# Kernel tuning notes

Measured on AMD Instinct MI355X. Metric: run time of the kernel, lower is better.

Reference implementation:

```python
import jax, jax.numpy as jnp
import numpy as np

B, Q, K, H = 8, 2048, 2048, 512


def setup_inputs() -> dict:
    key = jax.random.key(0)
    ks = jax.random.split(key, 12)
    s = 1.0 / np.sqrt(H)
    return {
        "query": jax.random.normal(ks[0], (B, Q, H), jnp.float32),
        "key_": jax.random.normal(ks[1], (B, K, H), jnp.float32),
        "value": jax.random.normal(ks[2], (B, K, H), jnp.float32),
        "mask": jax.random.randint(ks[3], (B, K), 0, 2).astype(bool),
        "Wq": jax.random.normal(ks[4], (H, H), jnp.float32) * s,
        "bq": jnp.zeros((H,), jnp.float32),
        "Wk": jax.random.normal(ks[5], (H, H), jnp.float32) * s,
        "bk": jnp.zeros((H,), jnp.float32),
        "Wv": jax.random.normal(ks[6], (H, H), jnp.float32) * s,
        "bv": jnp.zeros((H,), jnp.float32),
        "Wo": jax.random.normal(ks[7], (H, H), jnp.float32) * s,
        "bo": jnp.zeros((H,), jnp.float32),
    }


def reference(query, key_, value, mask, Wq, bq, Wk, bk, Wv, bv, Wo, bo):
    scale = jnp.sqrt(jnp.float32(H))
    Qp = query @ Wq + bq          # (B,Q,H)
    Kp = key_ @ Wk + bk           # (B,K,H)
    Vp = value @ Wv + bv          # (B,K,H)
    energy = jnp.einsum("bqh,bkh->bqk", Qp, Kp) / scale
    # mask is (B, key_len); torch code broadcasts it over all query rows
    energy = jnp.where(mask[:, None, :], -jnp.inf, energy)
    idx = jnp.argmax(energy, axis=-1)                 # (B,Q)
    score = jax.nn.one_hot(idx, K, dtype=energy.dtype)  # hardmax one-hot (B,Q,K)
    # score @ V is exactly a per-row gather of the argmax-selected V row
    res = jnp.take_along_axis(Vp, idx[:, :, None], axis=1)  # (B,Q,H)
    res = res @ Wo + bo
    return (res, score)
```

## Files before the change

kernel.cpp:

```cpp
#include <hip/hip_runtime.h>

typedef _Float16 f16;
typedef f16 f16x8 __attribute__((ext_vector_type(8)));
typedef f16 f16x4 __attribute__((ext_vector_type(4)));
typedef short s16x8 __attribute__((ext_vector_type(8)));
typedef short s16x4 __attribute__((ext_vector_type(4)));
typedef float f32x4 __attribute__((ext_vector_type(4)));

#define MFMA16(a,b,c)  __builtin_amdgcn_mfma_f32_16x16x32_f16(a,b,c,0,0,0)
#define MFMAB16(a,b,c) __builtin_amdgcn_mfma_f32_16x16x32_bf16(a,b,c,0,0,0)

static constexpr int Bn = 8, Qn = 2048, Kn = 2048, Hn = 512;
static constexpr int Mn = Bn * Qn;

typedef __attribute__((address_space(1))) const unsigned int as1_uint;
typedef __attribute__((address_space(3))) unsigned int as3_uint;

__device__ __forceinline__ void gl_lds16(const void* g, void* l) {
    __builtin_amdgcn_global_load_lds((as1_uint*)g, (as3_uint*)l, 16, 0, 0);
}

__device__ __forceinline__ short bf16r(float x) {
    unsigned u = __builtin_bit_cast(unsigned, x);
    u += 0x7fffu + ((u >> 16) & 1u);
    return (short)(u >> 16);
}

__device__ __forceinline__ int swz(int row) { return (row >> 1) & 3; }

__global__ __launch_bounds__(256) void compact_mask(
    const int* __restrict__ mask, int* __restrict__ cidx, int* __restrict__ cnt)
{
    __shared__ int sums[256];
    int b = blockIdx.x, t = threadIdx.x;
    int base = b * Kn + t * 8;
    int mv[8]; int s = 0;
    #pragma unroll
    for (int i = 0; i < 8; ++i) { mv[i] = (mask[base + i] == 0); s += mv[i]; }
    sums[t] = s;
    __syncthreads();
    for (int off = 1; off < 256; off <<= 1) {
        int v = (t >= off) ? sums[t - off] : 0;
        __syncthreads();
        sums[t] += v;
        __syncthreads();
    }
    int pos = (t > 0 ? sums[t - 1] : 0);
    #pragma unroll
    for (int i = 0; i < 8; ++i)
        if (mv[i]) cidx[b * Kn + pos++] = t * 8 + i;
    if (t == 255) {
        int total = sums[255];
        if (total == 0) { cidx[b * Kn] = 0; total = 1; }
        cnt[b] = total;
    }
}

__global__ __launch_bounds__(256) void prep_split(
    const float* __restrict__ Wk, const float* __restrict__ Wo,
    f16* __restrict__ Wk_h, f16* __restrict__ Wk_l, short* __restrict__ Wot)
{
    int e = blockIdx.x * 256 + threadIdx.x;
    float v = Wk[e] * 512.0f;
    f16 h = (f16)v;
    Wk_h[e] = h; Wk_l[e] = (f16)((v - (float)h) * 2048.0f);
    int r = e >> 9, c = e & 511;
    Wot[c * 512 + r] = bf16r(Wo[e]);
}

__global__ __launch_bounds__(512) void prep_vec(
    const float* __restrict__ Wk, const float* __restrict__ Wo,
    const float* __restrict__ bq, const float* __restrict__ bv,
    const float* __restrict__ bo,
    float* __restrict__ wvec, float* __restrict__ cvec)
{
    int t = threadIdx.x;
    float s = 0.f;
    for (int n = 0; n < 512; n += 4) {
        f32x4 a = *(const f32x4*)(Wk + (size_t)t * 512 + n);
        f32x4 q = *(const f32x4*)(bq + n);
        s += a[0]*q[0] + a[1]*q[1] + a[2]*q[2] + a[3]*q[3];
    }
    wvec[t] = s;
    float s2 = 0.f;
    for (int h = 0; h < 512; ++h) s2 += bv[h] * Wo[h * 512 + t];
    cvec[t] = s2 + bo[t];
}

template<int PREP>
__global__ __launch_bounds__(256) void gemm_split(
    const float* __restrict__ Af,
    const f16* __restrict__ Bh_g, const f16* __restrict__ Bl_g,
    f16* __restrict__ Oh, f16* __restrict__ Ol)
{
    __shared__ __align__(16) f16 Ah[2][2048], Al[2][2048], Bh[2][4096], Bl[2][4096];
    const int tid = threadIdx.x, lane = tid & 63, wid = tid >> 6;
    const int l15 = lane & 15, lg = lane >> 4;
    const int m0 = blockIdx.x * 64, n0 = blockIdx.y * 128;
    const int srow = lane >> 2, sg = lane & 3;
    const int ar0 = tid >> 3, ac0 = (tid & 7) * 4;

    auto stageB = [&](int buf, int ks) {
        const int k0 = ks << 5;
        #pragma unroll
        for (int h = 0; h < 2; ++h) {
            int s = wid + h * 4;
            int row = s * 16 + srow;
            int goff = k0 + ((sg ^ swz(row)) << 3);
            gl_lds16(Bh_g + (size_t)(n0 + row) * Hn + goff, &Bh[buf][s * 512]);
            gl_lds16(Bl_g + (size_t)(n0 + row) * Hn + goff, &Bl[buf][s * 512]);
        }
    };
    auto writeA = [&](int buf, const f32x4* av) {
        #pragma unroll
        for (int rr = 0; rr < 2; ++rr) {
            int row = ar0 + rr * 32;
            f16x4 oh, ol;
            #pragma unroll
            for (int j = 0; j < 4; ++j) {
                f16 hh = (f16)av[rr][j];
                oh[j] = hh;
                ol[j] = (f16)((av[rr][j] - (float)hh) * 2048.0f);
            }
            int off = row * 32 + (((ac0 >> 3) ^ swz(row)) << 3) + (ac0 & 7);
            *(f16x4*)&Ah[buf][off] = oh;
            *(f16x4*)&Al[buf][off] = ol;
        }
    };

    const float* aSrc[2];
    #pragma unroll
    for (int rr = 0; rr < 2; ++rr)
        aSrc[rr] = Af + (size_t)(m0 + ar0 + rr * 32) * Hn;

    f32x4 a0[4][2] = {}, a1[4][2] = {};
    {
        f32x4 av[2];
        #pragma unroll
        for (int rr = 0; rr < 2; ++rr) av[rr] = *(const f32x4*)(aSrc[rr] + ac0);
        stageB(0, 0);
        writeA(0, av);
    }
    __syncthreads();
    #pragma unroll 1
    for (int ks = 0; ks < 16; ++ks) {
        const int cur = ks & 1, nxt = cur ^ 1;
        f32x4 av[2];
        if (ks < 15) {
            const int k1 = (ks + 1) << 5;
            #pragma unroll
            for (int rr = 0; rr < 2; ++rr) av[rr] = *(const f32x4*)(aSrc[rr] + k1 + ac0);
            stageB(nxt, ks + 1);
        }
        f16x8 fbh[2], fbl[2];
        #pragma unroll
        for (int fj = 0; fj < 2; ++fj) {
            int row = wid * 32 + fj * 16 + l15;
            int off = row * 32 + ((lg ^ swz(row)) << 3);
            fbh[fj] = *(f16x8*)&Bh[cur][off];
            fbl[fj] = *(f16x8*)&Bl[cur][off];
        }
        #pragma unroll
        for (int fi = 0; fi < 4; ++fi) {
            int row = fi * 16 + l15;
            int off = row * 32 + ((lg ^ swz(row)) << 3);
            f16x8 fah = *(f16x8*)&Ah[cur][off];
            f16x8 fal = *(f16x8*)&Al[cur][off];
            #pragma unroll
            for (int fj = 0; fj < 2; ++fj) {
                a0[fi][fj] = MFMA16(fah, fbh[fj], a0[fi][fj]);
                a1[fi][fj] = MFMA16(fah, fbl[fj], a1[fi][fj]);
                a1[fi][fj] = MFMA16(fal, fbh[fj], a1[fi][fj]);
            }
        }
        if (ks < 15) writeA(nxt, av);
        __syncthreads();
    }
    #pragma unroll
    for (int fi = 0; fi < 4; ++fi)
    #pragma unroll
    for (int fj = 0; fj < 2; ++fj)
    #pragma unroll
    for (int j = 0; j < 4; ++j) {
        int m = m0 + fi * 16 + lg * 4 + j;
        int n = n0 + wid * 32 + fj * 16 + l15;
        float v = a0[fi][fj][j] + a1[fi][fj][j] * (1.0f / 2048.0f);
        if (PREP == 0) v *= (1.0f / 512.0f);
        f16 h = (f16)v;
        f16 lo = (f16)((v - (float)h) * 2048.0f);
        size_t o = PREP ? ((size_t)n * Hn + m) : ((size_t)m * Hn + n);
        Oh[o] = h; Ol[o] = lo;
    }
}

template<int MODE>
__global__ __launch_bounds__(256) void gemm_bfk(
    const float* __restrict__ Af, const short* __restrict__ Bt,
    const float* __restrict__ cvec, const int* __restrict__ idxArr,
    void* __restrict__ Out)
{
    __shared__ __align__(16) short As[2][2048], Bs[2][4096];
    const int tid = threadIdx.x, lane = tid & 63, wid = tid >> 6;
    const int l15 = lane & 15, lg = lane >> 4;
    const int m0 = blockIdx.x * 64, n0 = blockIdx.y * 128;
    const int srow = lane >> 2, sg = lane & 3;
    const int ar0 = tid >> 3, ac0 = (tid & 7) * 4;

    const float* aSrc[2];
    #pragma unroll
    for (int rr = 0; rr < 2; ++rr) {
        int row = ar0 + rr * 32;
        size_t grow;
        if (MODE == 1) {
            int b = m0 >> 11;
            grow = (size_t)(b * Kn + idxArr[m0 + row]);
        } else {
            grow = (size_t)(m0 + row);
        }
        aSrc[rr] = Af + grow * Hn;
    }

    auto stageB = [&](int buf, int ks) {
        const int k0 = ks << 5;
        #pragma unroll
        for (int h = 0; h < 2; ++h) {
            int s = wid + h * 4;
            int row = s * 16 + srow;
            int goff = k0 + ((sg ^ swz(row)) << 3);
            gl_lds16(Bt + (size_t)(n0 + row) * Hn + goff, &Bs[buf][s * 512]);
        }
    };
    auto writeA = [&](int buf, const f32x4* av) {
        #pragma unroll
        for (int rr = 0; rr < 2; ++rr) {
            int row = ar0 + rr * 32;
            s16x4 o;
            #pragma unroll
            for (int j = 0; j < 4; ++j) o[j] = bf16r(av[rr][j]);
            int off = row * 32 + (((ac0 >> 3) ^ swz(row)) << 3) + (ac0 & 7);
            *(s16x4*)&As[buf][off] = o;
        }
    };

    f32x4 acc[4][2] = {};
    {
        f32x4 av[2];
        #pragma unroll
        for (int rr = 0; rr < 2; ++rr) av[rr] = *(const f32x4*)(aSrc[rr] + ac0);
        stageB(0, 0);
        writeA(0, av);
    }
    __syncthreads();
    #pragma unroll 1
    for (int ks = 0; ks < 16; ++ks) {
        const int cur = ks & 1, nxt = cur ^ 1;
        f32x4 av[2];
        if (ks < 15) {
            const int k1 = (ks + 1) << 5;
            #pragma unroll
            for (int rr = 0; rr < 2; ++rr) av[rr] = *(const f32x4*)(aSrc[rr] + k1 + ac0);
            stageB(nxt, ks + 1);
        }
        s16x8 fb[2];
        #pragma unroll
        for (int fj = 0; fj < 2; ++fj) {
            int row = wid * 32 + fj * 16 + l15;
            fb[fj] = *(s16x8*)&Bs[cur][row * 32 + ((lg ^ swz(row)) << 3)];
        }
        #pragma unroll
        for (int fi = 0; fi < 4; ++fi) {
            int row = fi * 16 + l15;
            s16x8 fa = *(s16x8*)&As[cur][row * 32 + ((lg ^ swz(row)) << 3)];
            #pragma unroll
            for (int fj = 0; fj < 2; ++fj)
                acc[fi][fj] = MFMAB16(fa, fb[fj], acc[fi][fj]);
        }
        if (ks < 15) writeA(nxt, av);
        __syncthreads();
    }
    #pragma unroll
    for (int fi = 0; fi < 4; ++fi)
    #pragma unroll
    for (int fj = 0; fj < 2; ++fj)
    #pragma unroll
    for (int j = 0; j < 4; ++j) {
        int m = m0 + fi * 16 + lg * 4 + j;
        int n = n0 + wid * 32 + fj * 16 + l15;
        if (MODE == 0) {
            ((short*)Out)[(size_t)n * Hn + m] = bf16r(acc[fi][fj][j]);
        } else {
            ((float*)Out)[(size_t)m * Hn + n] = acc[fi][fj][j] + cvec[n];
        }
    }
}

__global__ __launch_bounds__(256) void kconv(
    const float* __restrict__ key_, const int* __restrict__ cidx,
    const int* __restrict__ cnt, const float* __restrict__ wvec,
    f16* __restrict__ Kc_h, f16* __restrict__ Kc_l, float* __restrict__ beta)
{
    int wid = threadIdx.x >> 6, lane = threadIdx.x & 63;
    int b = blockIdx.y, j = blockIdx.x * 4 + wid;
    int cn = cnt[b];
    if (j >= cn) return;
    const float* src = key_ + (size_t)(b * Kn + cidx[b * Kn + j]) * Hn;
    size_t dst = (size_t)(b * Kn + j) * Hn;
    float s = 0.f;
    #pragma unroll
    for (int i = 0; i < 2; ++i) {
        int c0 = lane * 8 + i * 4;
        f32x4 v = *(const f32x4*)(src + c0);
        f32x4 w = *(const f32x4*)(wvec + c0);
        f16x4 oh, ol;
        #pragma unroll
        for (int e = 0; e < 4; ++e) {
            f16 h = (f16)v[e];
            oh[e] = h;
            ol[e] = (f16)((v[e] - (float)h) * 2048.0f);
            s += v[e] * w[e];
        }
        *(f16x4*)(Kc_h + dst + c0) = oh;
        *(f16x4*)(Kc_l + dst + c0) = ol;
    }
    #pragma unroll
    for (int sm = 1; sm < 64; sm <<= 1) s += __shfl_xor(s, sm, 64);
    if (lane == 0) beta[b * Kn + j] = s;
}

__global__ __launch_bounds__(256) void energy_argmax(
    const f16* __restrict__ Qh, const f16* __restrict__ Ql,
    const f16* __restrict__ Kh, const f16* __restrict__ Kl,
    const float* __restrict__ beta, const int* __restrict__ cnt,
    float* __restrict__ pval, int* __restrict__ pidx)
{
    __shared__ __align__(16) f16 Ah[2][2048], Al[2][2048], Bh[2][4096], Bl[2][4096];
    const int tid = threadIdx.x, lane = tid & 63, wid = tid >> 6;
    const int l15 = lane & 15, lg = lane >> 4;
    const int qt = blockIdx.x, kc = blockIdx.y, b = blockIdx.z;
    const int cn = cnt[b];
    const int kbase = kc << 7;
    if (kbase >= cn) return;
    const int m0 = b * Qn + qt * 64;
    const int kr0 = b * Kn + kbase;
    const float NEGINF = -__builtin_inff();
    const int srow = lane >> 2, sg = lane & 3;

    auto stage = [&](int buf, int ks) {
        const int k0 = ks << 5;
        {
            int row = wid * 16 + srow;
            int goff = k0 + ((sg ^ swz(row)) << 3);
            size_t ga = (size_t)(m0 + row) * Hn + goff;
            gl_lds16(Qh + ga, &Ah[buf][wid * 512]);
            gl_lds16(Ql + ga, &Al[buf][wid * 512]);
        }
        #pragma unroll
        for (int h = 0; h < 2; ++h) {
            int s = wid + h * 4;
            int row = s * 16 + srow;
            int goff = k0 + ((sg ^ swz(row)) << 3);
            size_t gb = (size_t)(kr0 + row) * Hn + goff;
            gl_lds16(Kh + gb, &Bh[buf][s * 512]);
            gl_lds16(Kl + gb, &Bl[buf][s * 512]);
        }
    };

    f32x4 a0[4][2] = {}, a1[4][2] = {};
    stage(0, 0);
    __syncthreads();
    #pragma unroll 1
    for (int ks = 0; ks < 16; ++ks) {
        const int cur = ks & 1;
        if (ks < 15) stage(cur ^ 1, ks + 1);
        f16x8 fbh[2], fbl[2];
        #pragma unroll
        for (int fj = 0; fj < 2; ++fj) {
            int row = wid * 32 + fj * 16 + l15;
            int off = row * 32 + ((lg ^ swz(row)) << 3);
            fbh[fj] = *(f16x8*)&Bh[cur][off];
            fbl[fj] = *(f16x8*)&Bl[cur][off];
        }
        #pragma unroll
        for (int fi = 0; fi < 4; ++fi) {
            int row = fi * 16 + l15;
            int off = row * 32 + ((lg ^ swz(row)) << 3);
            f16x8 fah = *(f16x8*)&Ah[cur][off];
            f16x8 fal = *(f16x8*)&Al[cur][off];
            #pragma unroll
            for (int fj = 0; fj < 2; ++fj) {
                a0[fi][fj] = MFMA16(fah, fbh[fj], a0[fi][fj]);
                a1[fi][fj] = MFMA16(fah, fbl[fj], a1[fi][fj]);
                a1[fi][fj] = MFMA16(fal, fbh[fj], a1[fi][fj]);
            }
        }
        __syncthreads();
    }
    float (*bwv)[64] = (float(*)[64])&Ah[0][0];
    int   (*bwi)[64] = (int(*)[64])&Al[0][0];
    float bet[2];
    #pragma unroll
    for (int fj = 0; fj < 2; ++fj) {
        int lc = wid * 32 + fj * 16 + l15;
        bet[fj] = beta[b * Kn + kbase + lc];
    }
    #pragma unroll
    for (int fi = 0; fi < 4; ++fi) {
        #pragma unroll
        for (int j = 0; j < 4; ++j) {
            float bv = NEGINF; int bc = 0x7fffffff;
            #pragma unroll
            for (int fj = 0; fj < 2; ++fj) {
                int lc = wid * 32 + fj * 16 + l15;
                float v = a0[fi][fj][j] + a1[fi][fj][j] * (1.0f / 2048.0f) + bet[fj];
                v = (kbase + lc < cn) ? v : NEGINF;
                if (v > bv || (v == bv && lc < bc)) { bv = v; bc = lc; }
            }
            #pragma unroll
            for (int sm = 1; sm < 16; sm <<= 1) {
                float ov = __shfl_xor(bv, sm, 64);
                int   oc = __shfl_xor(bc, sm, 64);
                if (ov > bv || (ov == bv && oc < bc)) { bv = ov; bc = oc; }
            }
            if (l15 == 0) {
                int row = fi * 16 + lg * 4 + j;
                bwv[wid][row] = bv; bwi[wid][row] = bc;
            }
        }
    }
    __syncthreads();
    if (tid < 64) {
        float bv = bwv[0][tid]; int bc = bwi[0][tid];
        #pragma unroll
        for (int s = 1; s < 4; ++s) {
            float v = bwv[s][tid]; int i = bwi[s][tid];
            if (v > bv || (v == bv && i < bc)) { bv = v; bc = i; }
        }
        int m = m0 + tid;
        pval[m * 16 + kc] = bv;
        pidx[m * 16 + kc] = kbase + bc;
    }
}

__global__ __launch_bounds__(256) void merge(
    const float* __restrict__ pval, const int* __restrict__ pidx,
    const int* __restrict__ cnt, const int* __restrict__ cidx,
    int* __restrict__ idxArr)
{
    int m = blockIdx.x * 256 + threadIdx.x;
    int b = m >> 11;
    int nc = (cnt[b] + 127) >> 7;
    float bv = -__builtin_inff(); int bi = 0x7fffffff;
    for (int c = 0; c < nc; ++c) {
        float v = pval[m * 16 + c]; int i = pidx[m * 16 + c];
        if (v > bv || (v == bv && i < bi)) { bv = v; bi = i; }
    }
    idxArr[m] = cidx[b * Kn + bi];
}

__global__ __launch_bounds__(256) void score_fill(
    const int* __restrict__ idxArr, float* __restrict__ score)
{
    int m = blockIdx.x;
    int c = idxArr[m];
    float* row = score + (size_t)m * Kn;
    int t = threadIdx.x;
    #pragma unroll
    for (int i = 0; i < 2; ++i) {
        int v = t + i * 256;
        f32x4 val = {0.f, 0.f, 0.f, 0.f};
        if ((c >> 2) == v) val[c & 3] = 1.0f;
        *(f32x4*)(row + v * 4) = val;
    }
}

extern "C" void kernel_launch(void* const* d_in, const int* in_sizes, int n_in,
                              void* d_out, int out_size, void* d_ws, size_t ws_size,
                              hipStream_t stream)
{
    const float* query = (const float*)d_in[0];
    const float* key_  = (const float*)d_in[1];
    const float* value = (const float*)d_in[2];
    const int*   mask  = (const int*)d_in[3];
    const float* Wq = (const float*)d_in[4];
    const float* bq = (const float*)d_in[5];
    const float* Wk = (const float*)d_in[6];
    const float* bv = (const float*)d_in[9];
    const float* Wv = (const float*)d_in[8];
    const float* Wo = (const float*)d_in[10];
    const float* bo = (const float*)d_in[11];

    float* res = (float*)d_out;
    float* scoreBase = res + (size_t)Mn * Hn;
    char* sc = (char*)scoreBase;
    constexpr size_t MB = 1u << 20;
    f16*   qM_h = (f16*)(sc + 0 * MB);
    f16*   qM_l = (f16*)(sc + 16 * MB);
    f16*   Kc_h = (f16*)(sc + 32 * MB);
    f16*   Kc_l = (f16*)(sc + 48 * MB);
    f16*   Mt_h = (f16*)(sc + 64 * MB);
    f16*   Mt_l = (f16*)(sc + 64 * MB + 524288);
    f16*   Wk_h = (f16*)(sc + 65 * MB);
    f16*   Wk_l = (f16*)(sc + 65 * MB + 524288);
    short* Wot  = (short*)(sc + 66 * MB);
    short* NtB  = (short*)(sc + 66 * MB + 524288);
    float* wvec = (float*)(sc + 67 * MB);
    float* cvec = (float*)(sc + 67 * MB + 4096);
    float* beta = (float*)(sc + 67 * MB + 8192);
    float* pval = (float*)(sc + 67 * MB + 8192 + 65536);
    int*   pidx = (int*)(sc + 68 * MB + 8192 + 65536);
    int*   cidx = (int*)(sc + 69 * MB + 8192 + 65536);

    int*   idxArr = (int*)d_ws;
    int*   cnt    = (int*)d_ws + Mn;

    compact_mask<<<Bn, 256, 0, stream>>>(mask, cidx, cnt);
    prep_split<<<1024, 256, 0, stream>>>(Wk, Wo, Wk_h, Wk_l, Wot);
    prep_vec<<<1, 512, 0, stream>>>(Wk, Wo, bq, bv, bo, wvec, cvec);

    gemm_split<1><<<dim3(8, 4), 256, 0, stream>>>(Wq, Wk_h, Wk_l, Mt_h, Mt_l);
    gemm_bfk<0><<<dim3(8, 4), 256, 0, stream>>>(Wv, Wot, nullptr, nullptr, NtB);
    gemm_split<0><<<dim3(Mn / 64, 4), 256, 0, stream>>>(query, Mt_h, Mt_l, qM_h, qM_l);
    kconv<<<dim3(512, Bn), 256, 0, stream>>>(key_, cidx, cnt, wvec, Kc_h, Kc_l, beta);

    energy_argmax<<<dim3(Qn / 64, 16, Bn), 256, 0, stream>>>(
        qM_h, qM_l, Kc_h, Kc_l, beta, cnt, pval, pidx);

    merge<<<Mn / 256, 256, 0, stream>>>(pval, pidx, cnt, cidx, idxArr);

    gemm_bfk<1><<<dim3(Mn / 64, 4), 256, 0, stream>>>(value, NtB, cvec, idxArr, res);

    score_fill<<<Mn, 256, 0, stream>>>(idxArr, scoreBase);
}
```

Measured before the change: 288.3 us.

## Replace split-precision energy argmax with fp16 approximate energy plus candidate refinement

```diff
diff --git a/kernel.cpp b/kernel.cpp
--- a/kernel.cpp
+++ b/kernel.cpp
@@ -81,7 +81,7 @@
         f32x4 q = *(const f32x4*)(bq + n);
         s += a[0]*q[0] + a[1]*q[1] + a[2]*q[2] + a[3]*q[3];
     }
-    wvec[t] = s;
+    wvec[t] = s * (1.0f / 512.0f);
     float s2 = 0.f;
     for (int h = 0; h < 512; ++h) s2 += bv[h] * Wo[h * 512 + t];
     cvec[t] = s2 + bo[t];
@@ -297,7 +297,7 @@
 __global__ __launch_bounds__(256) void kconv(
     const float* __restrict__ key_, const int* __restrict__ cidx,
     const int* __restrict__ cnt, const float* __restrict__ wvec,
-    f16* __restrict__ Kc_h, f16* __restrict__ Kc_l, float* __restrict__ beta)
+    f16* __restrict__ Kc_h, float* __restrict__ beta)
 {
     int wid = threadIdx.x >> 6, lane = threadIdx.x & 63;
     int b = blockIdx.y, j = blockIdx.x * 4 + wid;
@@ -311,150 +311,172 @@
         int c0 = lane * 8 + i * 4;
         f32x4 v = *(const f32x4*)(src + c0);
         f32x4 w = *(const f32x4*)(wvec + c0);
-        f16x4 oh, ol;
+        f16x4 oh;
         #pragma unroll
         for (int e = 0; e < 4; ++e) {
-            f16 h = (f16)v[e];
-            oh[e] = h;
-            ol[e] = (f16)((v[e] - (float)h) * 2048.0f);
+            oh[e] = (f16)v[e];
             s += v[e] * w[e];
         }
         *(f16x4*)(Kc_h + dst + c0) = oh;
-        *(f16x4*)(Kc_l + dst + c0) = ol;
     }
     #pragma unroll
     for (int sm = 1; sm < 64; sm <<= 1) s += __shfl_xor(s, sm, 64);
     if (lane == 0) beta[b * Kn + j] = s;
 }
 
-__global__ __launch_bounds__(256) void energy_argmax(
-    const f16* __restrict__ Qh, const f16* __restrict__ Ql,
-    const f16* __restrict__ Kh, const f16* __restrict__ Kl,
+__global__ __launch_bounds__(256) void energy_approx(
+    const f16* __restrict__ Qh, const f16* __restrict__ Kh,
     const float* __restrict__ beta, const int* __restrict__ cnt,
-    float* __restrict__ pval, int* __restrict__ pidx)
-{
-    __shared__ __align__(16) f16 Ah[2][2048], Al[2][2048], Bh[2][4096], Bl[2][4096];
+    f16* __restrict__ approxE)
+{
+    __shared__ __align__(16) f16 Ah[2][4096], Bh[2][4096];
     const int tid = threadIdx.x, lane = tid & 63, wid = tid >> 6;
-    const int l15 = lane & 15, lg = lane >> 4;
+    const int wr = wid >> 1, wc = wid & 1, l15 = lane & 15, lg = lane >> 4;
     const int qt = blockIdx.x, kc = blockIdx.y, b = blockIdx.z;
     const int cn = cnt[b];
     const int kbase = kc << 7;
     if (kbase >= cn) return;
-    const int m0 = b * Qn + qt * 64;
+    const int m0 = b * Qn + qt * 128;
     const int kr0 = b * Kn + kbase;
-    const float NEGINF = -__builtin_inff();
     const int srow = lane >> 2, sg = lane & 3;
 
     auto stage = [&](int buf, int ks) {
         const int k0 = ks << 5;
-        {
-            int row = wid * 16 + srow;
-            int goff = k0 + ((sg ^ swz(row)) << 3);
-            size_t ga = (size_t)(m0 + row) * Hn + goff;
-            gl_lds16(Qh + ga, &Ah[buf][wid * 512]);
-            gl_lds16(Ql + ga, &Al[buf][wid * 512]);
-        }
         #pragma unroll
         for (int h = 0; h < 2; ++h) {
             int s = wid + h * 4;
             int row = s * 16 + srow;
             int goff = k0 + ((sg ^ swz(row)) << 3);
-            size_t gb = (size_t)(kr0 + row) * Hn + goff;
-            gl_lds16(Kh + gb, &Bh[buf][s * 512]);
-            gl_lds16(Kl + gb, &Bl[buf][s * 512]);
+            gl_lds16(Qh + (size_t)(m0 + row) * Hn + goff, &Ah[buf][s * 512]);
+            gl_lds16(Kh + (size_t)(kr0 + row) * Hn + goff, &Bh[buf][s * 512]);
         }
     };
 
-    f32x4 a0[4][2] = {}, a1[4][2] = {};
+    f32x4 acc[4][4] = {};
     stage(0, 0);
     __syncthreads();
     #pragma unroll 1
     for (int ks = 0; ks < 16; ++ks) {
         const int cur = ks & 1;
         if (ks < 15) stage(cur ^ 1, ks + 1);
-        f16x8 fbh[2], fbl[2];
-        #pragma unroll
-        for (int fj = 0; fj < 2; ++fj) {
-            int row = wid * 32 + fj * 16 + l15;
-            int off = row * 32 + ((lg ^ swz(row)) << 3);
-            fbh[fj] = *(f16x8*)&Bh[cur][off];
-            fbl[fj] = *(f16x8*)&Bl[cur][off];
+        f16x8 fb[4];
+        #pragma unroll
+        for (int fj = 0; fj < 4; ++fj) {
+            int row = wc * 64 + fj * 16 + l15;
+            fb[fj] = *(f16x8*)&Bh[cur][row * 32 + ((lg ^ swz(row)) << 3)];
         }
         #pragma unroll
         for (int fi = 0; fi < 4; ++fi) {
-            int row = fi * 16 + l15;
-            int off = row * 32 + ((lg ^ swz(row)) << 3);
-            f16x8 fah = *(f16x8*)&Ah[cur][off];
-            f16x8 fal = *(f16x8*)&Al[cur][off];
-            #pragma unroll
-            for (int fj = 0; fj < 2; ++fj) {
-                a0[fi][fj] = MFMA16(fah, fbh[fj], a0[fi][fj]);
-                a1[fi][fj] = MFMA16(fah, fbl[fj], a1[fi][fj]);
-                a1[fi][fj] = MFMA16(fal, fbh[fj], a1[fi][fj]);
+            int row = wr * 64 + fi * 16 + l15;
+            f16x8 fa = *(f16x8*)&Ah[cur][row * 32 + ((lg ^ swz(row)) << 3)];
+            #pragma unroll
+            for (int fj = 0; fj < 4; ++fj)
+                acc[fi][fj] = MFMA16(fa, fb[fj], acc[fi][fj]);
+        }
+        __syncthreads();
+    }
+    const f16 NEGI = (f16)(-__builtin_inff());
+    float bet[4]; int valid[4];
+    #pragma unroll
+    for (int fj = 0; fj < 4; ++fj) {
+        int lc = wc * 64 + fj * 16 + l15;
+        valid[fj] = (kbase + lc < cn);
+        bet[fj] = valid[fj] ? beta[b * Kn + kbase + lc] : 0.0f;
+    }
+    #pragma unroll
+    for (int fi = 0; fi < 4; ++fi)
+    #pragma unroll
+    for (int fj = 0; fj < 4; ++fj)
+    #pragma unroll
+    for (int j = 0; j < 4; ++j) {
+        int row = wr * 64 + fi * 16 + lg * 4 + j;
+        int col = wc * 64 + fj * 16 + l15;
+        f16 out = valid[fj] ? (f16)(acc[fi][fj][j] + bet[fj]) : NEGI;
+        approxE[(size_t)(m0 + row) * Kn + kbase + col] = out;
+    }
+}
+
+__global__ __launch_bounds__(256) void refine(
+    const f16* __restrict__ approxE,
+    const f16* __restrict__ qMh, const f16* __restrict__ qMl,
+    const float* __restrict__ key_, const float* __restrict__ beta,
+    const int* __restrict__ cidx, const int* __restrict__ cnt,
+    int* __restrict__ idxArr)
+{
+    const int wid = threadIdx.x >> 6, lane = threadIdx.x & 63;
+    const int m = blockIdx.x * 4 + wid;
+    const int b = m >> 11;
+    const int cn = cnt[b];
+    const int nc128 = ((cn + 127) >> 7) << 7;
+    const float NEGINF = -__builtin_inff();
+    const f16* row = approxE + (size_t)m * Kn;
+
+    f16x8 c[4];
+    float fmaxv = NEGINF;
+    #pragma unroll
+    for (int g = 0; g < 4; ++g) {
+        int cb = g * 512 + lane * 8;
+        if (cb < nc128) {
+            c[g] = *(const f16x8*)(row + cb);
+            #pragma unroll
+            for (int p = 0; p < 8; ++p) fmaxv = fmaxf(fmaxv, (float)c[g][p]);
+        } else {
+            #pragma unroll
+            for (int p = 0; p < 8; ++p) c[g][p] = (f16)NEGINF;
+        }
+    }
+    #pragma unroll
+    for (int sm = 1; sm < 64; sm <<= 1) fmaxv = fmaxf(fmaxv, __shfl_xor(fmaxv, sm, 64));
+    const float thr = fmaxv - 1.0f;
+
+    float q8[8];
+    int haveQ = 0;
+    float bestV = NEGINF; int bestOrig = 0x7fffffff;
+    int ncand = 0, firstJ = -1;
+
+    #pragma unroll
+    for (int g = 0; g < 4; ++g) {
+        #pragma unroll
+        for (int p = 0; p < 8; ++p) {
+            unsigned long long mb = __ballot((float)c[g][p] >= thr);
+            while (mb) {
+                int L = __builtin_ctzll(mb);
+                mb &= mb - 1;
+                int j = g * 512 + L * 8 + p;
+                ++ncand;
+                if (ncand == 1) { firstJ = j; continue; }
+                if (!haveQ) {
+                    haveQ = 1;
+                    int h0 = lane * 8;
+                    f16x8 qh = *(const f16x8*)(qMh + (size_t)m * Hn + h0);
+                    f16x8 ql = *(const f16x8*)(qMl + (size_t)m * Hn + h0);
+                    #pragma unroll
+                    for (int e = 0; e < 8; ++e)
+                        q8[e] = (float)qh[e] + (float)ql[e] * (1.0f / 2048.0f);
+                    int o1 = cidx[b * Kn + firstJ];
+                    const float* kr = key_ + ((size_t)(b * Kn + o1)) * Hn + lane * 8;
+                    float d = 0.f;
+                    #pragma unroll
+                    for (int e = 0; e < 8; ++e) d += q8[e] * kr[e];
+                    #pragma unroll
+                    for (int sm = 1; sm < 64; sm <<= 1) d += __shfl_xor(d, sm, 64);
+                    d += beta[b * Kn + firstJ];
+                    bestV = d; bestOrig = o1;
+                }
+                int orig = cidx[b * Kn + j];
+                const float* kr = key_ + ((size_t)(b * Kn + orig)) * Hn + lane * 8;
+                float d = 0.f;
+                #pragma unroll
+                for (int e = 0; e < 8; ++e) d += q8[e] * kr[e];
+                #pragma unroll
+                for (int sm = 1; sm < 64; sm <<= 1) d += __shfl_xor(d, sm, 64);
+                d += beta[b * Kn + j];
+                if (d > bestV || (d == bestV && orig < bestOrig)) { bestV = d; bestOrig = orig; }
             }
         }
-        __syncthreads();
-    }
-    float (*bwv)[64] = (float(*)[64])&Ah[0][0];
-    int   (*bwi)[64] = (int(*)[64])&Al[0][0];
-    float bet[2];
-    #pragma unroll
-    for (int fj = 0; fj < 2; ++fj) {
-        int lc = wid * 32 + fj * 16 + l15;
-        bet[fj] = beta[b * Kn + kbase + lc];
-    }
-    #pragma unroll
-    for (int fi = 0; fi < 4; ++fi) {
-        #pragma unroll
-        for (int j = 0; j < 4; ++j) {
-            float bv = NEGINF; int bc = 0x7fffffff;
-            #pragma unroll
-            for (int fj = 0; fj < 2; ++fj) {
-                int lc = wid * 32 + fj * 16 + l15;
-                float v = a0[fi][fj][j] + a1[fi][fj][j] * (1.0f / 2048.0f) + bet[fj];
-                v = (kbase + lc < cn) ? v : NEGINF;
-                if (v > bv || (v == bv && lc < bc)) { bv = v; bc = lc; }
-            }
-            #pragma unroll
-            for (int sm = 1; sm < 16; sm <<= 1) {
-                float ov = __shfl_xor(bv, sm, 64);
-                int   oc = __shfl_xor(bc, sm, 64);
-                if (ov > bv || (ov == bv && oc < bc)) { bv = ov; bc = oc; }
-            }
-            if (l15 == 0) {
-                int row = fi * 16 + lg * 4 + j;
-                bwv[wid][row] = bv; bwi[wid][row] = bc;
-            }
-        }
-    }
-    __syncthreads();
-    if (tid < 64) {
-        float bv = bwv[0][tid]; int bc = bwi[0][tid];
-        #pragma unroll
-        for (int s = 1; s < 4; ++s) {
-            float v = bwv[s][tid]; int i = bwi[s][tid];
-            if (v > bv || (v == bv && i < bc)) { bv = v; bc = i; }
-        }
-        int m = m0 + tid;
-        pval[m * 16 + kc] = bv;
-        pidx[m * 16 + kc] = kbase + bc;
-    }
-}
-
-__global__ __launch_bounds__(256) void merge(
-    const float* __restrict__ pval, const int* __restrict__ pidx,
-    const int* __restrict__ cnt, const int* __restrict__ cidx,
-    int* __restrict__ idxArr)
-{
-    int m = blockIdx.x * 256 + threadIdx.x;
-    int b = m >> 11;
-    int nc = (cnt[b] + 127) >> 7;
-    float bv = -__builtin_inff(); int bi = 0x7fffffff;
-    for (int c = 0; c < nc; ++c) {
-        float v = pval[m * 16 + c]; int i = pidx[m * 16 + c];
-        if (v > bv || (v == bv && i < bi)) { bv = v; bi = i; }
-    }
-    idxArr[m] = cidx[b * Kn + bi];
+    }
+    if (ncand == 1) bestOrig = cidx[b * Kn + firstJ];
+    if (lane == 0) idxArr[m] = bestOrig;
 }
 
 __global__ __launch_bounds__(256) void score_fill(
@@ -496,19 +518,18 @@
     f16*   qM_h = (f16*)(sc + 0 * MB);
     f16*   qM_l = (f16*)(sc + 16 * MB);
     f16*   Kc_h = (f16*)(sc + 32 * MB);
-    f16*   Kc_l = (f16*)(sc + 48 * MB);
-    f16*   Mt_h = (f16*)(sc + 64 * MB);
-    f16*   Mt_l = (f16*)(sc + 64 * MB + 524288);
-    f16*   Wk_h = (f16*)(sc + 65 * MB);
-    f16*   Wk_l = (f16*)(sc + 65 * MB + 524288);
-    short* Wot  = (short*)(sc + 66 * MB);
-    short* NtB  = (short*)(sc + 66 * MB + 524288);
-    float* wvec = (float*)(sc + 67 * MB);
-    float* cvec = (float*)(sc + 67 * MB + 4096);
-    float* beta = (float*)(sc + 67 * MB + 8192);
-    float* pval = (float*)(sc + 67 * MB + 8192 + 65536);
-    int*   pidx = (int*)(sc + 68 * MB + 8192 + 65536);
-    int*   cidx = (int*)(sc + 69 * MB + 8192 + 65536);
+    f16*   apxE = (f16*)(sc + 48 * MB);
+    char*  wb   = sc + 112 * MB;
+    f16*   Mt_h = (f16*)(wb);
+    f16*   Mt_l = (f16*)(wb + 524288);
+    f16*   Wk_h = (f16*)(wb + 2 * 524288);
+    f16*   Wk_l = (f16*)(wb + 3 * 524288);
+    short* Wot  = (short*)(wb + 4 * 524288);
+    short* NtB  = (short*)(wb + 5 * 524288);
+    float* wvec = (float*)(wb + 6 * 524288);
+    float* cvec = (float*)(wb + 6 * 524288 + 4096);
+    float* beta = (float*)(wb + 6 * 524288 + 8192);
+    int*   cidx = (int*)(wb + 6 * 524288 + 8192 + 65536);
 
     int*   idxArr = (int*)d_ws;
     int*   cnt    = (int*)d_ws + Mn;
@@ -520,12 +541,13 @@
     gemm_split<1><<<dim3(8, 4), 256, 0, stream>>>(Wq, Wk_h, Wk_l, Mt_h, Mt_l);
     gemm_bfk<0><<<dim3(8, 4), 256, 0, stream>>>(Wv, Wot, nullptr, nullptr, NtB);
     gemm_split<0><<<dim3(Mn / 64, 4), 256, 0, stream>>>(query, Mt_h, Mt_l, qM_h, qM_l);
-    kconv<<<dim3(512, Bn), 256, 0, stream>>>(key_, cidx, cnt, wvec, Kc_h, Kc_l, beta);
-
-    energy_argmax<<<dim3(Qn / 64, 16, Bn), 256, 0, stream>>>(
-        qM_h, qM_l, Kc_h, Kc_l, beta, cnt, pval, pidx);
-
-    merge<<<Mn / 256, 256, 0, stream>>>(pval, pidx, cnt, cidx, idxArr);
+    kconv<<<dim3(512, Bn), 256, 0, stream>>>(key_, cidx, cnt, wvec, Kc_h, beta);
+
+    energy_approx<<<dim3(Qn / 128, 16, Bn), 256, 0, stream>>>(
+        qM_h, Kc_h, beta, cnt, apxE);
+
+    refine<<<Mn / 4, 256, 0, stream>>>(
+        apxE, qM_h, qM_l, key_, beta, cidx, cnt, idxArr);
 
     gemm_bfk<1><<<dim3(Mn / 64, 4), 256, 0, stream>>>(value, NtB, cvec, idxArr, res);
 
```

After: 243.4 us. -15.6%, faster.
